# Optimization experiments

Hardware: AMD Instinct MI355X
Metric: run time of the kernel (lower is better)

## Reference

```python
import jax, jax.numpy as jnp
import numpy as np


def _cell(x, h, c, Wih, Whh, bih, bhh):
    # torch.nn.LSTMCell gate order: i, f, g, o
    gates = x @ Wih.T + h @ Whh.T + bih + bhh  # [B, 4H]
    i, f, g, o = jnp.split(gates, 4, axis=-1)
    i = jax.nn.sigmoid(i)
    f = jax.nn.sigmoid(f)
    g = jnp.tanh(g)
    o = jax.nn.sigmoid(o)
    c_new = f * c + i * g
    h_new = o * jnp.tanh(c_new)
    return h_new, c_new


def setup_inputs() -> dict:
    key = jax.random.key(0)
    B, T, D, H = 4096, 256, 4, 16
    ks = jax.random.split(key, 32)
    s = 1.0 / np.sqrt(H)  # torch LSTMCell/Linear uniform init bound

    def u(k, shape):
        return jax.random.uniform(k, shape, jnp.float32, -s, s)

    inp = {"y": jax.random.normal(ks[0], (B, T, D), jnp.float32)}
    names = ["f1", "f2", "f3", "b1", "b2", "b3"]
    ins = [D, H, H, D, H, H]
    idx = 1
    for n, di in zip(names, ins):
        inp[f"Wih_{n}"] = u(ks[idx], (4 * H, di)); idx += 1
        inp[f"Whh_{n}"] = u(ks[idx], (4 * H, H)); idx += 1
        inp[f"bih_{n}"] = u(ks[idx], (4 * H,)); idx += 1
        inp[f"bhh_{n}"] = u(ks[idx], (4 * H,)); idx += 1
    inp["W_out"] = u(ks[idx], (4, 2 * H)); idx += 1
    inp["b_out"] = u(ks[idx], (4,))
    return inp


def reference(y,
              Wih_f1, Whh_f1, bih_f1, bhh_f1,
              Wih_f2, Whh_f2, bih_f2, bhh_f2,
              Wih_f3, Whh_f3, bih_f3, bhh_f3,
              Wih_b1, Whh_b1, bih_b1, bhh_b1,
              Wih_b2, Whh_b2, bih_b2, bhh_b2,
              Wih_b3, Whh_b3, bih_b3, bhh_b3,
              W_out, b_out):
    B = y.shape[0]
    H = Whh_f1.shape[1]
    z = jnp.zeros((B, H), y.dtype)
    carry0 = (z, z, z, z, z, z, z, z, z, z, z, z)
    # forward-time and reversed-time sequences, time-major for scan: [T, B, 4]
    xs = (jnp.swapaxes(y, 0, 1), jnp.swapaxes(y[:, ::-1, :], 0, 1))

    def step(carry, x_t):
        hf1, cf1, hf2, cf2, hf3, cf3, hb1, cb1, hb2, cb2, hb3, cb3 = carry
        xf, xb = x_t
        hf1, cf1 = _cell(xf, hf1, cf1, Wih_f1, Whh_f1, bih_f1, bhh_f1)
        hf2, cf2 = _cell(hf1, hf2, cf2, Wih_f2, Whh_f2, bih_f2, bhh_f2)
        hf3, cf3 = _cell(hf2, hf3, cf3, Wih_f3, Whh_f3, bih_f3, bhh_f3)
        hb1, cb1 = _cell(xb, hb1, cb1, Wih_b1, Whh_b1, bih_b1, bhh_b1)
        hb2, cb2 = _cell(hb1, hb2, cb2, Wih_b2, Whh_b2, bih_b2, bhh_b2)
        hb3, cb3 = _cell(hb2, hb3, cb3, Wih_b3, Whh_b3, bih_b3, bhh_b3)
        return (hf1, cf1, hf2, cf2, hf3, cf3, hb1, cb1, hb2, cb2, hb3, cb3), None

    carry, _ = jax.lax.scan(step, carry0, xs)
    hf3, hb3 = carry[4], carry[10]
    out = jnp.concatenate([hf3, hb3], axis=1) @ W_out.T + b_out  # [B, 4]
    return out[:, None, :]  # [B, 1, 4]
```

## Files before the change

kernel.cpp:

```cpp
#include <hip/hip_runtime.h>

#define T_LEN 256
#define D_IN 4
#define SPR 8
#define NROUND (T_LEN / SPR + 2)

typedef __fp16 h8 __attribute__((ext_vector_type(8)));
typedef __fp16 cvt2_t __attribute__((ext_vector_type(2)));
typedef float float4v __attribute__((ext_vector_type(4)));

struct CellW { const float *Wih, *Whh, *bih, *bhh; };
struct Params { CellW c[6]; const float* y; float* hout; };

__device__ __forceinline__ float fexp2(float x) { return __builtin_amdgcn_exp2f(x); }
__device__ __forceinline__ float frcp(float x)  { return __builtin_amdgcn_rcpf(x); }
__device__ __forceinline__ int packh(float a, float b) {
    cvt2_t p = __builtin_amdgcn_cvt_pkrtz(a, b);
    return __builtin_bit_cast(int, p);
}
__device__ __forceinline__ h8 mk8(int a, int b, int c, int d) {
    int4 v; v.x = a; v.y = b; v.z = c; v.w = d;
    return __builtin_bit_cast(h8, v);
}

#define MFMA32(a, b, c) __builtin_amdgcn_mfma_f32_16x16x32_f16(a, b, c, 0, 0, 0)

__device__ __forceinline__ void act4(const float4v& pi, const float4v& pf,
                                     const float4v& pg, const float4v& po,
                                     float* cc, float* h) {
    float F[4], P[4], NG[4];
#pragma unroll
    for (int j = 0; j < 4; ++j) {
        float ei = fexp2(pi[j]);
        float ef = fexp2(pf[j]);
        float eg = fexp2(pg[j]);
        F[j]  = 1.f + ef;
        P[j]  = (1.f + ei) * (1.f + eg);
        NG[j] = 1.f - eg;
    }
    float RF01 = frcp(F[0] * F[1]);
    float RF23 = frcp(F[2] * F[3]);
    float RP01 = frcp(P[0] * P[1]);
    float RP23 = frcp(P[2] * P[3]);
    float f0 = RF01 * F[1], f1 = RF01 * F[0];
    float f2 = RF23 * F[3], f3 = RF23 * F[2];
    float ig0 = NG[0] * P[1] * RP01, ig1 = NG[1] * P[0] * RP01;
    float ig2 = NG[2] * P[3] * RP23, ig3 = NG[3] * P[2] * RP23;

    float NO[4], Dh[4];
    float cn0 = fmaf(f0, cc[0], ig0); cc[0] = cn0;
    float cn1 = fmaf(f1, cc[1], ig1); cc[1] = cn1;
    float cn2 = fmaf(f2, cc[2], ig2); cc[2] = cn2;
    float cn3 = fmaf(f3, cc[3], ig3); cc[3] = cn3;
    const float K2 = -2.8853900817779268f;
#pragma unroll
    for (int j = 0; j < 4; ++j) {
        float cn = cc[j];
        float eo = fexp2(po[j]);
        float ec = fexp2(fminf(cn * K2, 30.f));
        NO[j] = 1.f - ec;
        Dh[j] = (1.f + eo) * (1.f + ec);
    }
    float RH01 = frcp(Dh[0] * Dh[1]);
    float RH23 = frcp(Dh[2] * Dh[3]);
    h[0] = NO[0] * Dh[1] * RH01;
    h[1] = NO[1] * Dh[0] * RH01;
    h[2] = NO[2] * Dh[3] * RH23;
    h[3] = NO[3] * Dh[2] * RH23;
}

__global__ void __launch_bounds__(192)
__attribute__((amdgpu_waves_per_eu(1, 2)))
lstm_chain_kernel(Params p)
{
    __shared__ int2 lds_h[2][2][SPR][64];

    const int w = threadIdx.x >> 6;
    const int L = threadIdx.x & 63;
    const int n = L & 15;
    const int Q = L >> 4;

    const int tid = blockIdx.x;
    const int dir = tid & 1;
    const int b0  = (tid >> 1) * 16;

    const CellW cw = p.c[dir * 3 + w];
    const float LOG2E = 1.4426950408889634f;

    h8 A8[4];
    float4v bs[4];
#pragma unroll
    for (int g = 0; g < 4; ++g) {
        const float s = (g == 2) ? -2.f * LOG2E : -LOG2E;
        const int row = g * 16 + n;
        float vh[4], vp[4];
#pragma unroll
        for (int i = 0; i < 4; ++i) {
            const int k = 4 * Q + i;
            vh[i] = cw.Whh[row * 16 + k];
            vp[i] = (w == 0) ? ((Q == 0) ? cw.Wih[row * D_IN + k] : 0.f)
                             : cw.Wih[row * 16 + k];
        }
        A8[g] = mk8(packh(vh[0] * s, vh[1] * s), packh(vh[2] * s, vh[3] * s),
                    packh(vp[0] * s, vp[1] * s), packh(vp[2] * s, vp[3] * s));
        const int u0 = g * 16 + 4 * Q;
        float4 bi = *(const float4*)&cw.bih[u0];
        float4 bh = *(const float4*)&cw.bhh[u0];
        bs[g] = (float4v){(bi.x+bh.x)*s, (bi.y+bh.y)*s, (bi.z+bh.z)*s, (bi.w+bh.w)*s};
    }

    const float* ybase = p.y + (size_t)b0 * (T_LEN * D_IN);
    float4 xn[SPR];
    if (w == 0 && L < 16) {
#pragma unroll
        for (int k = 0; k < SPR; ++k) {
            const int tt = dir ? (T_LEN - 1 - k) : k;
            xn[k] = *(const float4*)(ybase + ((size_t)n * T_LEN + tt) * D_IN);
        }
    }

    float cc[4] = {0.f, 0.f, 0.f, 0.f};
    float h[4] = {0.f, 0.f, 0.f, 0.f};
    int hp0 = 0, hp1 = 0;

#pragma unroll 1
    for (int s = 0; s < NROUND; ++s) {
        __syncthreads();
        const int t0 = (s - w) * SPR;
        if (t0 < 0 || t0 >= T_LEN) continue;

        int xp[SPR][2];
        if (w == 0) {
            if (L < 16) {
#pragma unroll
                for (int k = 0; k < SPR; ++k) {
                    xp[k][0] = packh(xn[k].x, xn[k].y);
                    xp[k][1] = packh(xn[k].z, xn[k].w);
                }
                if (t0 + SPR < T_LEN) {
#pragma unroll
                    for (int k = 0; k < SPR; ++k) {
                        const int t = t0 + SPR + k;
                        const int tt = dir ? (T_LEN - 1 - t) : t;
                        xn[k] = *(const float4*)(ybase + ((size_t)n * T_LEN + tt) * D_IN);
                    }
                }
            } else {
#pragma unroll
                for (int k = 0; k < SPR; ++k) { xp[k][0] = 0; xp[k][1] = 0; }
            }
        }

        int2 hv[SPR];
        if (w >= 1) {
#pragma unroll
            for (int k = 0; k < SPR; ++k)
                hv[k] = lds_h[w - 1][(s + 1) & 1][k][L];
        }

#pragma unroll
        for (int k = 0; k < SPR; ++k) {
            const int pd0 = (w == 0) ? xp[k][0] : hv[k].x;
            const int pd1 = (w == 0) ? xp[k][1] : hv[k].y;
            const h8 b8 = mk8(hp0, hp1, pd0, pd1);
            float4v pi = MFMA32(A8[0], b8, bs[0]);
            float4v pf = MFMA32(A8[1], b8, bs[1]);
            float4v pg = MFMA32(A8[2], b8, bs[2]);
            float4v po = MFMA32(A8[3], b8, bs[3]);
            act4(pi, pf, pg, po, cc, h);
            hp0 = packh(h[0], h[1]);
            hp1 = packh(h[2], h[3]);
            if (w < 2) {
                int2 hw; hw.x = hp0; hw.y = hp1;
                lds_h[w][s & 1][k][L] = hw;
            }
        }
    }

    if (w == 2) {
        float4v ho = {h[0], h[1], h[2], h[3]};
        *(float4v*)&p.hout[(size_t)(b0 + n) * 32 + dir * 16 + 4 * Q] = ho;
    }
}

__global__ void out_proj_kernel(const float* __restrict__ ws,
                                const float* __restrict__ Wout,
                                const float* __restrict__ bout,
                                float* __restrict__ out, int B)
{
    int idx = blockIdx.x * blockDim.x + threadIdx.x;
    if (idx >= B * 4) return;
    int b = idx >> 2, o = idx & 3;
    float acc = bout[o];
    const float* h = ws + (size_t)b * 32;
    const float* w = Wout + o * 32;
#pragma unroll
    for (int m = 0; m < 32; ++m) acc = fmaf(h[m], w[m], acc);
    out[idx] = acc;
}

extern "C" void kernel_launch(void* const* d_in, const int* in_sizes, int n_in,
                              void* d_out, int out_size, void* d_ws, size_t ws_size,
                              hipStream_t stream)
{
    const int B = in_sizes[0] / (T_LEN * D_IN);

    Params p;
    for (int s = 0; s < 6; ++s) {
        p.c[s].Wih = (const float*)d_in[1 + 4 * s];
        p.c[s].Whh = (const float*)d_in[2 + 4 * s];
        p.c[s].bih = (const float*)d_in[3 + 4 * s];
        p.c[s].bhh = (const float*)d_in[4 + 4 * s];
    }
    p.y = (const float*)d_in[0];
    p.hout = (float*)d_ws;

    const int tiles = (B / 16) * 2;
    lstm_chain_kernel<<<tiles, 192, 0, stream>>>(p);

    const float* Wout = (const float*)d_in[25];
    const float* bout = (const float*)d_in[26];
    out_proj_kernel<<<(B * 4 + 255) / 256, 256, 0, stream>>>(
        (const float*)d_ws, Wout, bout, (float*)d_out, B);
}
```

Before: 273.8 us.

## Process two batch tiles per block to interleave independent LSTM recurrences

Each block now handles 32 batch rows as two independent 16-row tiles, issuing MFMAs and activations for both chains per timestep and using separate LDS handoff buffers. This gives instruction-level parallelism to hide the serial MFMA→activation latency of the recurrence, replacing co-resident waves. The grid halves and waves_per_eu is tightened to 1, so register pressure rises and per-CU occupancy falls.

```diff
diff --git a/kernel.cpp b/kernel.cpp
--- a/kernel.cpp
+++ b/kernel.cpp
@@ -48,16 +48,15 @@
     float ig2 = NG[2] * P[3] * RP23, ig3 = NG[3] * P[2] * RP23;
 
     float NO[4], Dh[4];
-    float cn0 = fmaf(f0, cc[0], ig0); cc[0] = cn0;
-    float cn1 = fmaf(f1, cc[1], ig1); cc[1] = cn1;
-    float cn2 = fmaf(f2, cc[2], ig2); cc[2] = cn2;
-    float cn3 = fmaf(f3, cc[3], ig3); cc[3] = cn3;
+    cc[0] = fmaf(f0, cc[0], ig0);
+    cc[1] = fmaf(f1, cc[1], ig1);
+    cc[2] = fmaf(f2, cc[2], ig2);
+    cc[3] = fmaf(f3, cc[3], ig3);
     const float K2 = -2.8853900817779268f;
 #pragma unroll
     for (int j = 0; j < 4; ++j) {
-        float cn = cc[j];
         float eo = fexp2(po[j]);
-        float ec = fexp2(fminf(cn * K2, 30.f));
+        float ec = fexp2(fminf(cc[j] * K2, 30.f));
         NO[j] = 1.f - ec;
         Dh[j] = (1.f + eo) * (1.f + ec);
     }
@@ -70,10 +69,11 @@
 }
 
 __global__ void __launch_bounds__(192)
-__attribute__((amdgpu_waves_per_eu(1, 2)))
+__attribute__((amdgpu_waves_per_eu(1, 1)))
 lstm_chain_kernel(Params p)
 {
-    __shared__ int2 lds_h[2][2][SPR][64];
+    __shared__ int2 lds_h0[2][2][SPR][64];
+    __shared__ int2 lds_h1[2][2][SPR][64];
 
     const int w = threadIdx.x >> 6;
     const int L = threadIdx.x & 63;
@@ -82,7 +82,7 @@
 
     const int tid = blockIdx.x;
     const int dir = tid & 1;
-    const int b0  = (tid >> 1) * 16;
+    const int b0  = (tid >> 1) * 32;
 
     const CellW cw = p.c[dir * 3 + w];
     const float LOG2E = 1.4426950408889634f;
@@ -109,19 +109,24 @@
         bs[g] = (float4v){(bi.x+bh.x)*s, (bi.y+bh.y)*s, (bi.z+bh.z)*s, (bi.w+bh.w)*s};
     }
 
-    const float* ybase = p.y + (size_t)b0 * (T_LEN * D_IN);
-    float4 xn[SPR];
+    const float* yb0 = p.y + (size_t)b0 * (T_LEN * D_IN);
+    const float* yb1 = p.y + (size_t)(b0 + 16) * (T_LEN * D_IN);
+    float4 xn0[SPR], xn1[SPR];
     if (w == 0 && L < 16) {
 #pragma unroll
         for (int k = 0; k < SPR; ++k) {
             const int tt = dir ? (T_LEN - 1 - k) : k;
-            xn[k] = *(const float4*)(ybase + ((size_t)n * T_LEN + tt) * D_IN);
-        }
-    }
-
-    float cc[4] = {0.f, 0.f, 0.f, 0.f};
-    float h[4] = {0.f, 0.f, 0.f, 0.f};
-    int hp0 = 0, hp1 = 0;
+            xn0[k] = *(const float4*)(yb0 + ((size_t)n * T_LEN + tt) * D_IN);
+            xn1[k] = *(const float4*)(yb1 + ((size_t)n * T_LEN + tt) * D_IN);
+        }
+    }
+
+    float cc0[4] = {0.f, 0.f, 0.f, 0.f};
+    float cc1[4] = {0.f, 0.f, 0.f, 0.f};
+    float h0[4] = {0.f, 0.f, 0.f, 0.f};
+    float h1[4] = {0.f, 0.f, 0.f, 0.f};
+    int hp00 = 0, hp01 = 0;
+    int hp10 = 0, hp11 = 0;
 
 #pragma unroll 1
     for (int s = 0; s < NROUND; ++s) {
@@ -129,57 +134,79 @@
         const int t0 = (s - w) * SPR;
         if (t0 < 0 || t0 >= T_LEN) continue;
 
-        int xp[SPR][2];
+        int xp0[SPR][2], xp1[SPR][2];
         if (w == 0) {
             if (L < 16) {
 #pragma unroll
                 for (int k = 0; k < SPR; ++k) {
-                    xp[k][0] = packh(xn[k].x, xn[k].y);
-                    xp[k][1] = packh(xn[k].z, xn[k].w);
+                    xp0[k][0] = packh(xn0[k].x, xn0[k].y);
+                    xp0[k][1] = packh(xn0[k].z, xn0[k].w);
+                    xp1[k][0] = packh(xn1[k].x, xn1[k].y);
+                    xp1[k][1] = packh(xn1[k].z, xn1[k].w);
                 }
                 if (t0 + SPR < T_LEN) {
 #pragma unroll
                     for (int k = 0; k < SPR; ++k) {
                         const int t = t0 + SPR + k;
                         const int tt = dir ? (T_LEN - 1 - t) : t;
-                        xn[k] = *(const float4*)(ybase + ((size_t)n * T_LEN + tt) * D_IN);
+                        xn0[k] = *(const float4*)(yb0 + ((size_t)n * T_LEN + tt) * D_IN);
+                        xn1[k] = *(const float4*)(yb1 + ((size_t)n * T_LEN + tt) * D_IN);
                     }
                 }
             } else {
 #pragma unroll
-                for (int k = 0; k < SPR; ++k) { xp[k][0] = 0; xp[k][1] = 0; }
+                for (int k = 0; k < SPR; ++k) {
+                    xp0[k][0] = 0; xp0[k][1] = 0;
+                    xp1[k][0] = 0; xp1[k][1] = 0;
+                }
             }
         }
 
-        int2 hv[SPR];
+        int2 hv0[SPR], hv1[SPR];
         if (w >= 1) {
 #pragma unroll
-            for (int k = 0; k < SPR; ++k)
-                hv[k] = lds_h[w - 1][(s + 1) & 1][k][L];
+            for (int k = 0; k < SPR; ++k) {
+                hv0[k] = lds_h0[w - 1][(s + 1) & 1][k][L];
+                hv1[k] = lds_h1[w - 1][(s + 1) & 1][k][L];
+            }
         }
 
 #pragma unroll
         for (int k = 0; k < SPR; ++k) {
-            const int pd0 = (w == 0) ? xp[k][0] : hv[k].x;
-            const int pd1 = (w == 0) ? xp[k][1] : hv[k].y;
-            const h8 b8 = mk8(hp0, hp1, pd0, pd1);
-            float4v pi = MFMA32(A8[0], b8, bs[0]);
-            float4v pf = MFMA32(A8[1], b8, bs[1]);
-            float4v pg = MFMA32(A8[2], b8, bs[2]);
-            float4v po = MFMA32(A8[3], b8, bs[3]);
-            act4(pi, pf, pg, po, cc, h);
-            hp0 = packh(h[0], h[1]);
-            hp1 = packh(h[2], h[3]);
+            const int pd00 = (w == 0) ? xp0[k][0] : hv0[k].x;
+            const int pd01 = (w == 0) ? xp0[k][1] : hv0[k].y;
+            const int pd10 = (w == 0) ? xp1[k][0] : hv1[k].x;
+            const int pd11 = (w == 0) ? xp1[k][1] : hv1[k].y;
+            const h8 b80 = mk8(hp00, hp01, pd00, pd01);
+            const h8 b81 = mk8(hp10, hp11, pd10, pd11);
+            float4v pi0 = MFMA32(A8[0], b80, bs[0]);
+            float4v pf0 = MFMA32(A8[1], b80, bs[1]);
+            float4v pg0 = MFMA32(A8[2], b80, bs[2]);
+            float4v po0 = MFMA32(A8[3], b80, bs[3]);
+            float4v pi1 = MFMA32(A8[0], b81, bs[0]);
+            float4v pf1 = MFMA32(A8[1], b81, bs[1]);
+            float4v pg1 = MFMA32(A8[2], b81, bs[2]);
+            float4v po1 = MFMA32(A8[3], b81, bs[3]);
+            act4(pi0, pf0, pg0, po0, cc0, h0);
+            act4(pi1, pf1, pg1, po1, cc1, h1);
+            hp00 = packh(h0[0], h0[1]);
+            hp01 = packh(h0[2], h0[3]);
+            hp10 = packh(h1[0], h1[1]);
+            hp11 = packh(h1[2], h1[3]);
             if (w < 2) {
-                int2 hw; hw.x = hp0; hw.y = hp1;
-                lds_h[w][s & 1][k][L] = hw;
+                int2 hw0; hw0.x = hp00; hw0.y = hp01;
+                int2 hw1; hw1.x = hp10; hw1.y = hp11;
+                lds_h0[w][s & 1][k][L] = hw0;
+                lds_h1[w][s & 1][k][L] = hw1;
             }
         }
     }
 
     if (w == 2) {
-        float4v ho = {h[0], h[1], h[2], h[3]};
-        *(float4v*)&p.hout[(size_t)(b0 + n) * 32 + dir * 16 + 4 * Q] = ho;
+        float4v ho0 = {h0[0], h0[1], h0[2], h0[3]};
+        float4v ho1 = {h1[0], h1[1], h1[2], h1[3]};
+        *(float4v*)&p.hout[(size_t)(b0 + n) * 32 + dir * 16 + 4 * Q] = ho0;
+        *(float4v*)&p.hout[(size_t)(b0 + 16 + n) * 32 + dir * 16 + 4 * Q] = ho1;
     }
 }
 
@@ -215,7 +242,7 @@
     p.y = (const float*)d_in[0];
     p.hout = (float*)d_ws;
 
-    const int tiles = (B / 16) * 2;
+    const int tiles = (B / 32) * 2;
     lstm_chain_kernel<<<tiles, 192, 0, stream>>>(p);
 
     const float* Wout = (const float*)d_in[25];
```

New measurement: 279.4 us. 1.02x slower.

## Split input and recurrent MFMAs to take input projection off the serial chain

Applied to the files above, without the earlier changes.

Replaces the single 16x16x32 MFMA per gate (which mixed the h and x/h-below operands) with two 16x16x16 MFMAs. The input-side projection is precomputed two steps ahead into a double buffer of accumulators, so only the recurrent Whh MFMA sits on the time-step dependency chain. The activation math is also reworked to merge the forget and input/gate reciprocals into one shared reciprocal for the cell update. This issues more MFMA instructions and holds more live accumulator registers. The combined-fraction form of the cell update may also lose some numerical robustness.

```diff
diff --git a/kernel.cpp b/kernel.cpp
--- a/kernel.cpp
+++ b/kernel.cpp
@@ -5,7 +5,7 @@
 #define SPR 8
 #define NROUND (T_LEN / SPR + 2)
 
-typedef __fp16 h8 __attribute__((ext_vector_type(8)));
+typedef __fp16 h4 __attribute__((ext_vector_type(4)));
 typedef __fp16 cvt2_t __attribute__((ext_vector_type(2)));
 typedef float float4v __attribute__((ext_vector_type(4)));
 
@@ -18,17 +18,17 @@
     cvt2_t p = __builtin_amdgcn_cvt_pkrtz(a, b);
     return __builtin_bit_cast(int, p);
 }
-__device__ __forceinline__ h8 mk8(int a, int b, int c, int d) {
-    int4 v; v.x = a; v.y = b; v.z = c; v.w = d;
-    return __builtin_bit_cast(h8, v);
-}
-
-#define MFMA32(a, b, c) __builtin_amdgcn_mfma_f32_16x16x32_f16(a, b, c, 0, 0, 0)
+__device__ __forceinline__ h4 mk(int lo, int hi) {
+    int2 v; v.x = lo; v.y = hi;
+    return __builtin_bit_cast(h4, v);
+}
+
+#define MFMA16(a, b, c) __builtin_amdgcn_mfma_f32_16x16x16f16(a, b, c, 0, 0, 0)
 
 __device__ __forceinline__ void act4(const float4v& pi, const float4v& pf,
                                      const float4v& pg, const float4v& po,
                                      float* cc, float* h) {
-    float F[4], P[4], NG[4];
+    float F[4], P[4], NG[4], den[4], num[4];
 #pragma unroll
     for (int j = 0; j < 4; ++j) {
         float ei = fexp2(pi[j]);
@@ -37,27 +37,22 @@
         F[j]  = 1.f + ef;
         P[j]  = (1.f + ei) * (1.f + eg);
         NG[j] = 1.f - eg;
-    }
-    float RF01 = frcp(F[0] * F[1]);
-    float RF23 = frcp(F[2] * F[3]);
-    float RP01 = frcp(P[0] * P[1]);
-    float RP23 = frcp(P[2] * P[3]);
-    float f0 = RF01 * F[1], f1 = RF01 * F[0];
-    float f2 = RF23 * F[3], f3 = RF23 * F[2];
-    float ig0 = NG[0] * P[1] * RP01, ig1 = NG[1] * P[0] * RP01;
-    float ig2 = NG[2] * P[3] * RP23, ig3 = NG[3] * P[2] * RP23;
-
+        den[j] = F[j] * P[j];
+        num[j] = fmaf(cc[j], P[j], NG[j] * F[j]);
+    }
+    float RC01 = frcp(den[0] * den[1]);
+    float RC23 = frcp(den[2] * den[3]);
+    cc[0] = num[0] * den[1] * RC01;
+    cc[1] = num[1] * den[0] * RC01;
+    cc[2] = num[2] * den[3] * RC23;
+    cc[3] = num[3] * den[2] * RC23;
+
+    const float K2 = -2.8853900817779268f;
     float NO[4], Dh[4];
-    float cn0 = fmaf(f0, cc[0], ig0); cc[0] = cn0;
-    float cn1 = fmaf(f1, cc[1], ig1); cc[1] = cn1;
-    float cn2 = fmaf(f2, cc[2], ig2); cc[2] = cn2;
-    float cn3 = fmaf(f3, cc[3], ig3); cc[3] = cn3;
-    const float K2 = -2.8853900817779268f;
 #pragma unroll
     for (int j = 0; j < 4; ++j) {
-        float cn = cc[j];
         float eo = fexp2(po[j]);
-        float ec = fexp2(fminf(cn * K2, 30.f));
+        float ec = fexp2(fminf(cc[j] * K2, 30.f));
         NO[j] = 1.f - ec;
         Dh[j] = (1.f + eo) * (1.f + ec);
     }
@@ -87,22 +82,22 @@
     const CellW cw = p.c[dir * 3 + w];
     const float LOG2E = 1.4426950408889634f;
 
-    h8 A8[4];
+    h4 Aih[4], Ahh[4];
     float4v bs[4];
 #pragma unroll
     for (int g = 0; g < 4; ++g) {
         const float s = (g == 2) ? -2.f * LOG2E : -LOG2E;
         const int row = g * 16 + n;
-        float vh[4], vp[4];
+        float vi[4], vh[4];
 #pragma unroll
         for (int i = 0; i < 4; ++i) {
             const int k = 4 * Q + i;
+            vi[i] = (w == 0) ? ((Q == 0) ? cw.Wih[row * D_IN + k] : 0.f)
+                             : cw.Wih[row * 16 + k];
             vh[i] = cw.Whh[row * 16 + k];
-            vp[i] = (w == 0) ? ((Q == 0) ? cw.Wih[row * D_IN + k] : 0.f)
-                             : cw.Wih[row * 16 + k];
-        }
-        A8[g] = mk8(packh(vh[0] * s, vh[1] * s), packh(vh[2] * s, vh[3] * s),
-                    packh(vp[0] * s, vp[1] * s), packh(vp[2] * s, vp[3] * s));
+        }
+        Aih[g] = mk(packh(vi[0] * s, vi[1] * s), packh(vi[2] * s, vi[3] * s));
+        Ahh[g] = mk(packh(vh[0] * s, vh[1] * s), packh(vh[2] * s, vh[3] * s));
         const int u0 = g * 16 + 4 * Q;
         float4 bi = *(const float4*)&cw.bih[u0];
         float4 bh = *(const float4*)&cw.bhh[u0];
@@ -129,13 +124,13 @@
         const int t0 = (s - w) * SPR;
         if (t0 < 0 || t0 >= T_LEN) continue;
 
-        int xp[SPR][2];
+        int2 bv[SPR];
         if (w == 0) {
             if (L < 16) {
 #pragma unroll
                 for (int k = 0; k < SPR; ++k) {
-                    xp[k][0] = packh(xn[k].x, xn[k].y);
-                    xp[k][1] = packh(xn[k].z, xn[k].w);
+                    bv[k].x = packh(xn[k].x, xn[k].y);
+                    bv[k].y = packh(xn[k].z, xn[k].w);
                 }
                 if (t0 + SPR < T_LEN) {
 #pragma unroll
@@ -147,26 +142,35 @@
                 }
             } else {
 #pragma unroll
-                for (int k = 0; k < SPR; ++k) { xp[k][0] = 0; xp[k][1] = 0; }
+                for (int k = 0; k < SPR; ++k) { bv[k].x = 0; bv[k].y = 0; }
             }
-        }
-
-        int2 hv[SPR];
-        if (w >= 1) {
+        } else {
 #pragma unroll
             for (int k = 0; k < SPR; ++k)
-                hv[k] = lds_h[w - 1][(s + 1) & 1][k][L];
+                bv[k] = lds_h[w - 1][(s + 1) & 1][k][L];
+        }
+
+        float4v pre[2][4];
+#pragma unroll
+        for (int g = 0; g < 4; ++g) {
+            pre[0][g] = MFMA16(Aih[g], mk(bv[0].x, bv[0].y), bs[g]);
+            pre[1][g] = MFMA16(Aih[g], mk(bv[1].x, bv[1].y), bs[g]);
         }
 
 #pragma unroll
         for (int k = 0; k < SPR; ++k) {
-            const int pd0 = (w == 0) ? xp[k][0] : hv[k].x;
-            const int pd1 = (w == 0) ? xp[k][1] : hv[k].y;
-            const h8 b8 = mk8(hp0, hp1, pd0, pd1);
-            float4v pi = MFMA32(A8[0], b8, bs[0]);
-            float4v pf = MFMA32(A8[1], b8, bs[1]);
-            float4v pg = MFMA32(A8[2], b8, bs[2]);
-            float4v po = MFMA32(A8[3], b8, bs[3]);
+            const h4 bh = mk(hp0, hp1);
+            float4v pi = MFMA16(Ahh[0], bh, pre[k & 1][0]);
+            float4v pf = MFMA16(Ahh[1], bh, pre[k & 1][1]);
+            float4v pg = MFMA16(Ahh[2], bh, pre[k & 1][2]);
+            float4v po = MFMA16(Ahh[3], bh, pre[k & 1][3]);
+            if (k + 2 < SPR) {
+                const h4 bn = mk(bv[k + 2].x, bv[k + 2].y);
+                pre[k & 1][0] = MFMA16(Aih[0], bn, bs[0]);
+                pre[k & 1][1] = MFMA16(Aih[1], bn, bs[1]);
+                pre[k & 1][2] = MFMA16(Aih[2], bn, bs[2]);
+                pre[k & 1][3] = MFMA16(Aih[3], bn, bs[3]);
+            }
             act4(pi, pf, pg, po, cc, h);
             hp0 = packh(h[0], h[1]);
             hp1 = packh(h[2], h[3]);
```

Result: no change. 274.3 us (+0.2%).

## Double timesteps per round, fuse cell-state reciprocals, pre-pack prefetched inputs

Applied to the files above, without the earlier changes.

Raises the number of timesteps handled between block barriers from 8 to 16, halving the number of synchronisation rounds in the layer wavefront pipeline. The wavefront fill adds two extra rounds, so each extra round now costs more steps of pipeline skew. The activation math is rewritten so the new cell state comes from one combined numerator/denominator with a shared reciprocal, instead of separate reciprocals for the forget gate and the input-times-candidate term, cutting rcp and multiply work on the serial recurrence path. The prefetched inputs are packed to fp16 right after loading, so fewer registers hold them, and the per-step operand selects are merged into one buffer.

```diff
diff --git a/kernel.cpp b/kernel.cpp
--- a/kernel.cpp
+++ b/kernel.cpp
@@ -2,7 +2,7 @@
 
 #define T_LEN 256
 #define D_IN 4
-#define SPR 8
+#define SPR 16
 #define NROUND (T_LEN / SPR + 2)
 
 typedef __fp16 h8 __attribute__((ext_vector_type(8)));
@@ -28,7 +28,7 @@
 __device__ __forceinline__ void act4(const float4v& pi, const float4v& pf,
                                      const float4v& pg, const float4v& po,
                                      float* cc, float* h) {
-    float F[4], P[4], NG[4];
+    float F[4], P[4], NG[4], den[4], num[4];
 #pragma unroll
     for (int j = 0; j < 4; ++j) {
         float ei = fexp2(pi[j]);
@@ -37,27 +37,22 @@
         F[j]  = 1.f + ef;
         P[j]  = (1.f + ei) * (1.f + eg);
         NG[j] = 1.f - eg;
-    }
-    float RF01 = frcp(F[0] * F[1]);
-    float RF23 = frcp(F[2] * F[3]);
-    float RP01 = frcp(P[0] * P[1]);
-    float RP23 = frcp(P[2] * P[3]);
-    float f0 = RF01 * F[1], f1 = RF01 * F[0];
-    float f2 = RF23 * F[3], f3 = RF23 * F[2];
-    float ig0 = NG[0] * P[1] * RP01, ig1 = NG[1] * P[0] * RP01;
-    float ig2 = NG[2] * P[3] * RP23, ig3 = NG[3] * P[2] * RP23;
-
+        den[j] = F[j] * P[j];
+        num[j] = fmaf(cc[j], P[j], NG[j] * F[j]);
+    }
+    float RC01 = frcp(den[0] * den[1]);
+    float RC23 = frcp(den[2] * den[3]);
+    cc[0] = num[0] * den[1] * RC01;
+    cc[1] = num[1] * den[0] * RC01;
+    cc[2] = num[2] * den[3] * RC23;
+    cc[3] = num[3] * den[2] * RC23;
+
+    const float K2 = -2.8853900817779268f;
     float NO[4], Dh[4];
-    float cn0 = fmaf(f0, cc[0], ig0); cc[0] = cn0;
-    float cn1 = fmaf(f1, cc[1], ig1); cc[1] = cn1;
-    float cn2 = fmaf(f2, cc[2], ig2); cc[2] = cn2;
-    float cn3 = fmaf(f3, cc[3], ig3); cc[3] = cn3;
-    const float K2 = -2.8853900817779268f;
 #pragma unroll
     for (int j = 0; j < 4; ++j) {
-        float cn = cc[j];
         float eo = fexp2(po[j]);
-        float ec = fexp2(fminf(cn * K2, 30.f));
+        float ec = fexp2(fminf(cc[j] * K2, 30.f));
         NO[j] = 1.f - ec;
         Dh[j] = (1.f + eo) * (1.f + ec);
     }
@@ -110,12 +105,14 @@
     }
 
     const float* ybase = p.y + (size_t)b0 * (T_LEN * D_IN);
-    float4 xn[SPR];
+    int2 xn[SPR];
     if (w == 0 && L < 16) {
 #pragma unroll
         for (int k = 0; k < SPR; ++k) {
             const int tt = dir ? (T_LEN - 1 - k) : k;
-            xn[k] = *(const float4*)(ybase + ((size_t)n * T_LEN + tt) * D_IN);
+            float4 t = *(const float4*)(ybase + ((size_t)n * T_LEN + tt) * D_IN);
+            xn[k].x = packh(t.x, t.y);
+            xn[k].y = packh(t.z, t.w);
         }
     }
 
@@ -129,40 +126,34 @@
         const int t0 = (s - w) * SPR;
         if (t0 < 0 || t0 >= T_LEN) continue;
 
-        int xp[SPR][2];
+        int2 bv[SPR];
         if (w == 0) {
             if (L < 16) {
 #pragma unroll
-                for (int k = 0; k < SPR; ++k) {
-                    xp[k][0] = packh(xn[k].x, xn[k].y);
-                    xp[k][1] = packh(xn[k].z, xn[k].w);
-                }
+                for (int k = 0; k < SPR; ++k) bv[k] = xn[k];
                 if (t0 + SPR < T_LEN) {
 #pragma unroll
                     for (int k = 0; k < SPR; ++k) {
                         const int t = t0 + SPR + k;
                         const int tt = dir ? (T_LEN - 1 - t) : t;
-                        xn[k] = *(const float4*)(ybase + ((size_t)n * T_LEN + tt) * D_IN);
+                        float4 x = *(const float4*)(ybase + ((size_t)n * T_LEN + tt) * D_IN);
+                        xn[k].x = packh(x.x, x.y);
+                        xn[k].y = packh(x.z, x.w);
                     }
                 }
             } else {
 #pragma unroll
-                for (int k = 0; k < SPR; ++k) { xp[k][0] = 0; xp[k][1] = 0; }
+                for (int k = 0; k < SPR; ++k) { bv[k].x = 0; bv[k].y = 0; }
             }
-        }
-
-        int2 hv[SPR];
-        if (w >= 1) {
+        } else {
 #pragma unroll
             for (int k = 0; k < SPR; ++k)
-                hv[k] = lds_h[w - 1][(s + 1) & 1][k][L];
+                bv[k] = lds_h[w - 1][(s + 1) & 1][k][L];
         }
 
 #pragma unroll
         for (int k = 0; k < SPR; ++k) {
-            const int pd0 = (w == 0) ? xp[k][0] : hv[k].x;
-            const int pd1 = (w == 0) ? xp[k][1] : hv[k].y;
-            const h8 b8 = mk8(hp0, hp1, pd0, pd1);
+            const h8 b8 = mk8(hp0, hp1, bv[k].x, bv[k].y);
             float4v pi = MFMA32(A8[0], b8, bs[0]);
             float4v pf = MFMA32(A8[1], b8, bs[1]);
             float4v pg = MFMA32(A8[2], b8, bs[2]);
```

Measured after the change: 270.7 us. Within noise of the previous version (-1.1%).
